# Performance work log

Measured on AMD Instinct MI355X. Metric: run time of the kernel, lower is better.

## Reference

```python
import jax, jax.numpy as jnp
import numpy as np

N, E, G = 50000, 800000, 64          # nodes, edges, graphs in batch
F, HG, HL = 64, 128, 128             # node feat, graph hidden, lin hidden
AVG_LOG = float(np.log(9.0))         # from deg histogram [0]*8+[1]: log(8+1)


def setup_inputs() -> dict:
    key = jax.random.key(0)
    ks = jax.random.split(key, 24)
    def w(k, shape):
        return 0.1 * jax.random.normal(k, shape, jnp.float32)
    return {
        "x": jax.random.normal(ks[0], (N, F), jnp.float32),
        "edge_index": jax.random.randint(ks[1], (2, E), 0, N),
        "edge_attr": jax.random.normal(ks[2], (E, 1), jnp.float32),
        "batch": jnp.sort(jax.random.randint(ks[3], (N,), 0, G)),
        # PNAConv params (towers=1, pre_layers=1, post_layers=1, edge_dim=1)
        "W_edge": w(ks[4], (1, F)),      "b_edge": w(ks[5], (F,)),
        "W_pre": w(ks[6], (3 * F, F)),   "b_pre": w(ks[7], (F,)),
        "W_post": w(ks[8], (13 * F, HG)), "b_post": w(ks[9], (HG,)),
        "W_lin": w(ks[10], (HG, HG)),    "b_lin": w(ks[11], (HG,)),
        # bn1 / fc2 / bn2
        "g1": jnp.ones((HG,)), "be1": jnp.zeros((HG,)),
        "W2": w(ks[12], (HG, HL)), "b2": w(ks[13], (HL,)),
        "g2": jnp.ones((HL,)), "be2": jnp.zeros((HL,)),
        # one resnet block: fc/bn/fc/bn
        "Wr1": w(ks[14], (HL, HL)), "br1": w(ks[15], (HL,)),
        "gr1": jnp.ones((HL,)), "ber1": jnp.zeros((HL,)),
        "Wr2": w(ks[16], (HL, HL)), "br2": w(ks[17], (HL,)),
        "gr2": jnp.ones((HL,)), "ber2": jnp.zeros((HL,)),
        "W_out": w(ks[18], (HL, 1)), "b_out": w(ks[19], (1,)),
    }


def _bn(z, g, b):
    # BatchNorm1d, training mode: biased batch stats, eps=1e-5
    mu = z.mean(0)
    var = ((z - mu) ** 2).mean(0)
    return (z - mu) * jax.lax.rsqrt(var + 1e-5) * g + b


def _pna(x, edge_index, edge_attr, W_edge, b_edge, W_pre, b_pre,
         W_post, b_post, W_lin, b_lin):
    src, dst = edge_index[0], edge_index[1]  # messages flow j->i, aggregate at dst
    e = edge_attr @ W_edge + b_edge                               # [E, F]
    m = jnp.concatenate([x[dst], x[src], e], -1) @ W_pre + b_pre  # [E, F]
    ones_e = jnp.ones((m.shape[0],), m.dtype)
    cnt = jax.ops.segment_sum(ones_e, dst, N)                     # in-degree
    cnt1 = jnp.maximum(cnt, 1.0)
    mean = jax.ops.segment_sum(m, dst, N) / cnt1[:, None]
    mean2 = jax.ops.segment_sum(m * m, dst, N) / cnt1[:, None]
    std = jnp.sqrt(jax.nn.relu(mean2 - mean * mean) + 1e-5)
    has = (cnt > 0)[:, None]
    mn = jnp.where(has, jax.ops.segment_min(m, dst, N), 0.0)
    mx = jnp.where(has, jax.ops.segment_max(m, dst, N), 0.0)
    agg = jnp.concatenate([mean, mn, mx, std], -1)                # [N, 4F]
    amp = (jnp.log(cnt1 + 1.0) / AVG_LOG)[:, None]                # amplification scaler
    out = jnp.concatenate([agg, agg * amp, agg / amp], -1)        # [N, 12F]
    out = jnp.concatenate([x, out], -1) @ W_post + b_post         # [N, HG]
    return out @ W_lin + b_lin                                    # [N, HG]


def reference(x, edge_index, edge_attr, batch,
              W_edge, b_edge, W_pre, b_pre, W_post, b_post, W_lin, b_lin,
              g1, be1, W2, b2, g2, be2,
              Wr1, br1, gr1, ber1, Wr2, br2, gr2, ber2,
              W_out, b_out):
    h = _pna(x, edge_index, edge_attr, W_edge, b_edge, W_pre, b_pre,
             W_post, b_post, W_lin, b_lin)
    # global_mean_pool over graphs
    gc = jnp.maximum(jax.ops.segment_sum(jnp.ones((h.shape[0],), h.dtype), batch, G), 1.0)
    z = jax.ops.segment_sum(h, batch, G) / gc[:, None]            # [G, HG]
    z = jax.nn.relu(_bn(z, g1, be1))
    z = jax.nn.relu(_bn(z @ W2 + b2, g2, be2))
    r = z
    z = jax.nn.relu(_bn(z @ Wr1 + br1, gr1, ber1))
    z = jax.nn.relu(_bn(z @ Wr2 + br2, gr2, ber2) + r)
    return z @ W_out + b_out                                      # [G, 1]
```

## Files before the change

kernel.cpp:

```cpp
#include <hip/hip_runtime.h>
#include <hip/hip_bf16.h>

using bf16 = __hip_bfloat16;

#define F 64
#define HG 128
#define HL 128
#define AVG_LOG_INV 0.45511961331341866f
#define BSH 5
#define BNODES 32
#define BCAP 1024
#define BTILE 8192
#define NBMAX 1664

typedef short short8 __attribute__((ext_vector_type(8)));
typedef float floatx4 __attribute__((ext_vector_type(4)));

__device__ __forceinline__ float b2f(bf16 v) { return __bfloat162float(v); }
__device__ __forceinline__ bf16 f2b(float v) { return __float2bfloat16(v); }
__device__ __forceinline__ short f2bs(float v) { bf16 h = f2b(v); return *(short*)&h; }

__device__ __forceinline__ unsigned packbf2(float x, float y) {
    bf16 a = f2b(x), b = f2b(y);
    unsigned short ua = *(unsigned short*)&a, ub = *(unsigned short*)&b;
    return ((unsigned)ub << 16) | (unsigned)ua;
}

__device__ __forceinline__ float wave_sum(float v) {
    #pragma unroll
    for (int m = 32; m > 0; m >>= 1) v += __shfl_xor(v, m);
    return v;
}

__global__ void k_ab_mfma(const float* __restrict__ x, const float* __restrict__ W_pre,
                          bf16* __restrict__ AB, int N,
                          int* __restrict__ gcur, float* __restrict__ gfeat,
                          int* __restrict__ gcnt, int NB, int GF, int G,
                          const float* __restrict__ W_edge, const float* __restrict__ b_edge,
                          const float* __restrict__ b_pre, float* __restrict__ uc) {
    int gtid = blockIdx.x * blockDim.x + threadIdx.x;
    int gstr = gridDim.x * blockDim.x;
    for (int i = gtid; i < GF; i += gstr) gfeat[i] = 0.f;
    for (int i = gtid; i < NB; i += gstr) gcur[i] = 0;
    for (int i = gtid; i < G; i += gstr) gcnt[i] = 0;
    if (blockIdx.x == 0 && threadIdx.x < 64) {
        int f = threadIdx.x;
        float u = 0.f, c = b_pre[f];
        for (int k = 0; k < 64; k++) {
            float w3 = W_pre[(128 + k) * 64 + f];
            u += W_edge[k] * w3;
            c += b_edge[k] * w3;
        }
        uc[f] = u; uc[64 + f] = c;
    }

    __shared__ unsigned short wt[128 * 72];
    for (int idx = threadIdx.x; idx < 8192; idx += 256) {
        int k = idx >> 7, m = idx & 127;
        float v = W_pre[((m & 64) + k) * 64 + (m & 63)];
        wt[m * 72 + k] = (unsigned short)f2bs(v);
    }
    __syncthreads();

    int lane = threadIdx.x & 63;
    int row = lane & 15, quad = lane >> 4;
    int w = (blockIdx.x * blockDim.x + threadIdx.x) >> 6;
    int nwaves = (gridDim.x * blockDim.x) >> 6;
    int ntiles = (N + 15) >> 4;

    for (int tile = w; tile < ntiles; tile += nwaves) {
        int m0 = tile << 4;
        int node_a = m0 + row; if (node_a >= N) node_a = N - 1;
        short8 a[2];
        #pragma unroll
        for (int h = 0; h < 2; h++) {
            const float* xp = x + (size_t)node_a * 64 + h * 32 + quad * 8;
            floatx4 v0 = *(const floatx4*)xp;
            floatx4 v1 = *(const floatx4*)(xp + 4);
            #pragma unroll
            for (int j = 0; j < 4; j++) { a[h][j] = f2bs(v0[j]); a[h][4 + j] = f2bs(v1[j]); }
        }
        #pragma unroll
        for (int t = 0; t < 8; t++) {
            int fbase = t * 16;
            floatx4 c = {0.f, 0.f, 0.f, 0.f};
            #pragma unroll
            for (int h = 0; h < 2; h++) {
                short8 b = *(const short8*)(wt + (fbase + row) * 72 + h * 32 + quad * 8);
                c = __builtin_amdgcn_mfma_f32_16x16x32_bf16(a[h], b, c, 0, 0, 0);
            }
            #pragma unroll
            for (int r = 0; r < 4; r++) {
                int node = m0 + quad * 4 + r;
                if (node < N) AB[(size_t)node * 128 + fbase + row] = f2b(c[r]);
            }
        }
    }
}

__global__ void k_bucket(const int* __restrict__ ei, const float* __restrict__ ea,
                         int* __restrict__ gcur, int2* __restrict__ gout,
                         int E, int NB) {
    __shared__ int2 recs[BTILE];
    __shared__ int hist[NBMAX], gst[NBMAX], lrk[NBMAX];
    int t = threadIdx.x;
    for (int b = t; b < NB; b += 1024) hist[b] = 0;
    __syncthreads();
    int base = blockIdx.x * BTILE;
    int lim = E - base; if (lim > BTILE) lim = BTILE;
    int nq = lim >> 2;
    const int4* src4 = (const int4*)(ei + base);
    const int4* dst4 = (const int4*)(ei + E + base);
    const float4* ea4 = (const float4*)(ea + base);
    for (int q = t; q < nq; q += 1024) {
        int4 s = src4[q], d = dst4[q];
        float4 v = ea4[q];
        int i = q * 4;
        recs[i]     = make_int2((d.x << 16) | s.x, __float_as_int(v.x));
        recs[i + 1] = make_int2((d.y << 16) | s.y, __float_as_int(v.y));
        recs[i + 2] = make_int2((d.z << 16) | s.z, __float_as_int(v.z));
        recs[i + 3] = make_int2((d.w << 16) | s.w, __float_as_int(v.w));
        atomicAdd(&hist[d.x >> BSH], 1);
        atomicAdd(&hist[d.y >> BSH], 1);
        atomicAdd(&hist[d.z >> BSH], 1);
        atomicAdd(&hist[d.w >> BSH], 1);
    }
    for (int i = (nq << 2) + t; i < lim; i += 1024) {
        int e = base + i;
        int src = ei[e], dst = ei[E + e];
        recs[i] = make_int2((dst << 16) | src, __float_as_int(ea[e]));
        atomicAdd(&hist[dst >> BSH], 1);
    }
    __syncthreads();
    for (int b = t; b < NB; b += 1024) {
        int h = hist[b];
        lrk[b] = 0;
        gst[b] = (h > 0) ? atomicAdd(&gcur[b], h) : 0;
    }
    __syncthreads();
    for (int i = t; i < lim; i += 1024) {
        int2 r = recs[i];
        int b = ((unsigned)r.x) >> (16 + BSH);
        int k = atomicAdd(&lrk[b], 1);
        int pos = gst[b] + k;
        if (pos < BCAP) gout[(size_t)b * BCAP + pos] = r;
    }
}

__global__ void k_edge(const bf16* __restrict__ AB, const int2* __restrict__ gout,
                       const int* __restrict__ gcur, const float* __restrict__ uc,
                       const int* __restrict__ batch, float* __restrict__ gfeat,
                       int N) {
    __shared__ int2 recs[BCAP], sortd[BCAP];
    __shared__ int ncnt[BNODES], nofs[BNODES], nrank[BNODES];
    __shared__ int gid[BNODES];
    __shared__ unsigned lstat[BNODES][128];
    __shared__ float lamp[BNODES], liamp[BNODES];
    int t = threadIdx.x;
    int b = blockIdx.x;
    int nn = N - b * BNODES; if (nn > BNODES) nn = BNODES;
    int ecnt = gcur[b]; if (ecnt > BCAP) ecnt = BCAP;

    for (int i = t; i < ecnt; i += 512) recs[i] = gout[(size_t)b * BCAP + i];
    if (t < BNODES) {
        ncnt[t] = 0; nrank[t] = 0;
        if (t < nn) gid[t] = batch[b * BNODES + t];
    }
    __syncthreads();
    for (int i = t; i < ecnt; i += 512)
        atomicAdd(&ncnt[((unsigned)recs[i].x >> 16) & (BNODES - 1)], 1);
    __syncthreads();
    if (t < BNODES) {
        int v = ncnt[t], inc = v;
        #pragma unroll
        for (int m = 1; m < BNODES; m <<= 1) { int u = __shfl_up(inc, m); if (t >= m) inc += u; }
        nofs[t] = inc - v;
    }
    __syncthreads();
    for (int i = t; i < ecnt; i += 512) {
        int2 r = recs[i];
        int nl = ((unsigned)r.x >> 16) & (BNODES - 1);
        int k = atomicAdd(&nrank[nl], 1);
        sortd[nofs[nl] + k] = r;
    }
    __syncthreads();

    int lane = t & 63, w = t >> 6;
    int half = lane & 31, hi32 = lane >> 5;
    float2 u2 = *(const float2*)(uc + 2 * half);
    float2 c2 = *(const float2*)(uc + 64 + 2 * half);

    for (int nl = w; nl < nn; nl += 8) {
        int n = b * BNODES + nl;
        int lo = nofs[nl], cnt = ncnt[nl], hi = lo + cnt;

        unsigned apack = *(const unsigned*)(AB + (size_t)n * 128 + 2 * half);
        float acx = __uint_as_float(apack << 16) + c2.x;
        float acy = __uint_as_float(apack & 0xffff0000u) + c2.y;

        float sx = 0.f, sy = 0.f, qx = 0.f, qy = 0.f;
        float mnx = 3.4e38f, mny = 3.4e38f, mxx = -3.4e38f, mxy = -3.4e38f;

        auto acc2 = [&](unsigned bp, float eav) {
            float bx = __uint_as_float(bp << 16);
            float by = __uint_as_float(bp & 0xffff0000u);
            float m0 = fmaf(eav, u2.x, acx) + bx;
            float m1 = fmaf(eav, u2.y, acy) + by;
            sx += m0; qx = fmaf(m0, m0, qx);
            sy += m1; qy = fmaf(m1, m1, qy);
            mnx = fminf(mnx, m0); mxx = fmaxf(mxx, m0);
            mny = fminf(mny, m1); mxy = fmaxf(mxy, m1);
        };
        auto gaddr = [&](int sn) {
            return (const unsigned*)(AB + (size_t)sn * 128 + 64 + 2 * half);
        };

        for (int base = lo; base < hi; base += 64) {
            int nb = hi - base; if (nb > 64) nb = 64;
            int2 rec = (lane < nb) ? sortd[base + lane] : make_int2(0, 0);
            int vsn = rec.x & 0xFFFF;
            float vea = __int_as_float(rec.y);
            int i = 0;
            for (; i + 8 <= nb; i += 8) {
                int sn0 = __shfl(vsn, i + hi32);
                int sn1 = __shfl(vsn, i + 2 + hi32);
                int sn2 = __shfl(vsn, i + 4 + hi32);
                int sn3 = __shfl(vsn, i + 6 + hi32);
                float e0 = __shfl(vea, i + hi32);
                float e1 = __shfl(vea, i + 2 + hi32);
                float e2 = __shfl(vea, i + 4 + hi32);
                float e3 = __shfl(vea, i + 6 + hi32);
                unsigned b0 = *gaddr(sn0);
                unsigned b1 = *gaddr(sn1);
                unsigned b2 = *gaddr(sn2);
                unsigned b3 = *gaddr(sn3);
                acc2(b0, e0); acc2(b1, e1); acc2(b2, e2); acc2(b3, e3);
            }
            for (; i + 2 <= nb; i += 2) {
                int   sn = __shfl(vsn, i + hi32);
                float ev = __shfl(vea, i + hi32);
                acc2(*gaddr(sn), ev);
            }
            if (i < nb) {
                int   sn = __shfl(vsn, i);
                float ev = __shfl(vea, i);
                unsigned bp = *gaddr(sn);
                if (hi32 == 0) acc2(bp, ev);
            }
        }
        sx += __shfl_xor(sx, 32); sy += __shfl_xor(sy, 32);
        qx += __shfl_xor(qx, 32); qy += __shfl_xor(qy, 32);
        mnx = fminf(mnx, __shfl_xor(mnx, 32)); mny = fminf(mny, __shfl_xor(mny, 32));
        mxx = fmaxf(mxx, __shfl_xor(mxx, 32)); mxy = fmaxf(mxy, __shfl_xor(mxy, 32));

        float c1 = (cnt > 0) ? (float)cnt : 1.f;
        float inv = 1.f / c1;
        float mex = sx * inv, mey = sy * inv;
        float vx = qx * inv - mex * mex; if (vx < 0.f) vx = 0.f;
        float vy = qy * inv - mey * mey; if (vy < 0.f) vy = 0.f;
        float sdx = sqrtf(vx + 1e-5f), sdy = sqrtf(vy + 1e-5f);
        if (cnt == 0) { mnx = mny = mxx = mxy = 0.f; }

        if (hi32 == 0) {
            lstat[nl][half]      = packbf2(mex, mey);
            lstat[nl][32 + half] = packbf2(mnx, mny);
        } else {
            lstat[nl][64 + half] = packbf2(mxx, mxy);
            lstat[nl][96 + half] = packbf2(sdx, sdy);
        }
        if (lane == 0) {
            float amp = logf(c1 + 1.f) * AVG_LOG_INV;
            lamp[nl] = amp; liamp[nl] = 1.f / amp;
        }
    }
    __syncthreads();

    if (t < 128) {
        int c = t;
        int elem = ((c >> 5) << 6) + ((c & 31) << 1);
        float s1x = 0.f, s1y = 0.f, s2x = 0.f, s2y = 0.f, s3x = 0.f, s3y = 0.f;
        int cur = gid[0];
        for (int nl = 0; nl < nn; nl++) {
            int g = gid[nl];
            if (g != cur) {
                float* gf = gfeat + (size_t)cur * 832;
                unsafeAtomicAdd(&gf[64 + elem], s1x);
                unsafeAtomicAdd(&gf[65 + elem], s1y);
                unsafeAtomicAdd(&gf[320 + elem], s2x);
                unsafeAtomicAdd(&gf[321 + elem], s2y);
                unsafeAtomicAdd(&gf[576 + elem], s3x);
                unsafeAtomicAdd(&gf[577 + elem], s3y);
                s1x = s1y = s2x = s2y = s3x = s3y = 0.f;
                cur = g;
            }
            unsigned p = lstat[nl][c];
            float bx = __uint_as_float(p << 16);
            float by = __uint_as_float(p & 0xffff0000u);
            float a = lamp[nl], ia = liamp[nl];
            s1x += bx; s2x = fmaf(bx, a, s2x); s3x = fmaf(bx, ia, s3x);
            s1y += by; s2y = fmaf(by, a, s2y); s3y = fmaf(by, ia, s3y);
        }
        float* gf = gfeat + (size_t)cur * 832;
        unsafeAtomicAdd(&gf[64 + elem], s1x);
        unsafeAtomicAdd(&gf[65 + elem], s1y);
        unsafeAtomicAdd(&gf[320 + elem], s2x);
        unsafeAtomicAdd(&gf[321 + elem], s2y);
        unsafeAtomicAdd(&gf[576 + elem], s3x);
        unsafeAtomicAdd(&gf[577 + elem], s3y);
    }
}

__global__ void k_gx(const float* __restrict__ x, const int* __restrict__ batch,
                     float* __restrict__ gfeat, int* __restrict__ gcnt,
                     int N, int chunk) {
    int t = threadIdx.x;
    int lo = blockIdx.x * chunk;
    int hi = lo + chunk; if (hi > N) hi = N;
    if (lo >= hi) return;
    int curg = batch[lo];
    float sx = 0.f;
    int cnt = 0;
    for (int n = lo; n < hi; n++) {
        int g = batch[n];
        if (g != curg) {
            unsafeAtomicAdd(&gfeat[(size_t)curg * 832 + t], sx);
            if (t == 0) atomicAdd(&gcnt[curg], cnt);
            sx = 0.f; cnt = 0; curg = g;
        }
        sx += x[(size_t)n * 64 + t];
        cnt++;
    }
    unsafeAtomicAdd(&gfeat[(size_t)curg * 832 + t], sx);
    if (t == 0) atomicAdd(&gcnt[curg], cnt);
}

__global__ void k_post1(const float* __restrict__ gfeat, const int* __restrict__ gcnt,
                        const float* __restrict__ W_post, const float* __restrict__ b_post,
                        const float* __restrict__ W_lin, const float* __restrict__ b_lin,
                        float* __restrict__ Zin) {
    int g = blockIdx.x, j = threadIdx.x;
    __shared__ float feat[832];
    __shared__ float z1[128];
    int cg = gcnt[g];
    float r = 1.f / ((cg > 0) ? (float)cg : 1.f);
    for (int i = j; i < 832; i += 128) feat[i] = gfeat[(size_t)g * 832 + i] * r;
    __syncthreads();
    float acc = b_post[j];
    for (int k = 0; k < 832; k++) acc += feat[k] * W_post[k * 128 + j];
    z1[j] = acc;
    __syncthreads();
    float a2 = b_lin[j];
    for (int k = 0; k < 128; k++) a2 += z1[k] * W_lin[k * 128 + j];
    if (cg == 0) a2 = 0.f;
    Zin[g * 128 + j] = a2;
}

__global__ void k_mlpcol(const float* __restrict__ in, const float* __restrict__ W,
                         const float* __restrict__ bias,
                         const float* __restrict__ gamma, const float* __restrict__ beta,
                         const float* __restrict__ res,
                         const float* __restrict__ g_in, const float* __restrict__ be_in,
                         float* __restrict__ outp) {
    __shared__ float A[64 * 129];
    __shared__ float part[4 * 64];
    int t = threadIdx.x;
    int j = blockIdx.x;

    for (int i = t; i < 8192; i += 256) A[(i >> 7) * 129 + (i & 127)] = in[i];
    __syncthreads();

    if (g_in) {
        if (t < 128) {
            int c = t;
            float mu = 0.f;
            for (int r = 0; r < 64; r++) mu += A[r * 129 + c];
            mu *= (1.f / 64.f);
            float var = 0.f;
            for (int r = 0; r < 64; r++) { float d = A[r * 129 + c] - mu; var += d * d; }
            var *= (1.f / 64.f);
            float sc = rsqrtf(var + 1e-5f) * g_in[c], sh = be_in[c];
            for (int r = 0; r < 64; r++) {
                float v = (A[r * 129 + c] - mu) * sc + sh;
                A[r * 129 + c] = v > 0.f ? v : 0.f;
            }
        }
        __syncthreads();
    }

    int r = t & 63, q = t >> 6;
    float acc = 0.f;
    int k0 = q * 32;
    #pragma unroll
    for (int k = 0; k < 32; k++) acc += A[r * 129 + k0 + k] * W[(k0 + k) * 128 + j];
    part[q * 64 + r] = acc;
    __syncthreads();

    if (t < 64) {
        float v = part[t] + part[64 + t] + part[128 + t] + part[192 + t] + bias[j];
        float mu = wave_sum(v) * (1.f / 64.f);
        float d = v - mu;
        float var = wave_sum(d * d) * (1.f / 64.f);
        float o = d * rsqrtf(var + 1e-5f) * gamma[j] + beta[j];
        if (res) o += res[t * 128 + j];
        outp[t * 128 + j] = o > 0.f ? o : 0.f;
    }
}

__global__ void k_out(const float* __restrict__ z4, const float* __restrict__ W_out,
                      const float* b_out, float* __restrict__ out) {
    int g = threadIdx.x;
    float acc = b_out[0];
    for (int j = 0; j < 128; j++) acc += z4[g * 128 + j] * W_out[j];
    out[g] = acc;
}

extern "C" void kernel_launch(void* const* d_in, const int* in_sizes, int n_in,
                              void* d_out, int out_size, void* d_ws, size_t ws_size,
                              hipStream_t stream) {
    const float* x      = (const float*)d_in[0];
    const int*   ei     = (const int*)d_in[1];
    const float* ea     = (const float*)d_in[2];
    const int*   batch  = (const int*)d_in[3];
    const float* W_edge = (const float*)d_in[4];
    const float* b_edge = (const float*)d_in[5];
    const float* W_pre  = (const float*)d_in[6];
    const float* b_pre  = (const float*)d_in[7];
    const float* W_post = (const float*)d_in[8];
    const float* b_post = (const float*)d_in[9];
    const float* W_lin  = (const float*)d_in[10];
    const float* b_lin  = (const float*)d_in[11];
    const float* g1     = (const float*)d_in[12];
    const float* be1    = (const float*)d_in[13];
    const float* W2     = (const float*)d_in[14];
    const float* b2     = (const float*)d_in[15];
    const float* g2     = (const float*)d_in[16];
    const float* be2    = (const float*)d_in[17];
    const float* Wr1    = (const float*)d_in[18];
    const float* br1    = (const float*)d_in[19];
    const float* gr1    = (const float*)d_in[20];
    const float* ber1   = (const float*)d_in[21];
    const float* Wr2    = (const float*)d_in[22];
    const float* br2    = (const float*)d_in[23];
    const float* gr2    = (const float*)d_in[24];
    const float* ber2   = (const float*)d_in[25];
    const float* W_out  = (const float*)d_in[26];
    const float* b_out  = (const float*)d_in[27];
    float* out = (float*)d_out;

    const int N = in_sizes[0] / F;
    const int E = in_sizes[1] / 2;
    const int G = out_size;
    const int NB = (N + BNODES - 1) >> BSH;

    char* p = (char*)d_ws;
    auto alloc = [&](size_t nbytes) { void* r = p; p += (nbytes + 255) & ~(size_t)255; return r; };
    bf16*  AB     = (bf16*)alloc((size_t)N * 128 * sizeof(bf16));
    int*   gcur   = (int*)alloc((size_t)NB * sizeof(int));
    int2*  gout   = (int2*)alloc((size_t)NB * BCAP * sizeof(int2));
    float* uc     = (float*)alloc(128 * sizeof(float));
    float* gfeat  = (float*)alloc((size_t)G * 832 * sizeof(float));
    int*   gcnt   = (int*)alloc((size_t)G * sizeof(int));
    float* Zin    = (float*)alloc(64 * 128 * sizeof(float));
    float* z2b    = (float*)alloc(64 * 128 * sizeof(float));
    float* z3b    = (float*)alloc(64 * 128 * sizeof(float));
    float* z4b    = (float*)alloc(64 * 128 * sizeof(float));

    const int GF = G * 832;
    const int GXB = 2048;
    const int GXCH = (N + GXB - 1) / GXB;
    const int ABB = ((N + 15) / 16 + 3) / 4;
    const int NBT = (E + BTILE - 1) / BTILE;

    k_ab_mfma<<<ABB, 256, 0, stream>>>(x, W_pre, AB, N, gcur, gfeat, gcnt, NB, GF, G,
                                       W_edge, b_edge, b_pre, uc);
    k_bucket<<<NBT, 1024, 0, stream>>>(ei, ea, gcur, gout, E, NB);
    k_edge<<<NB, 512, 0, stream>>>(AB, gout, gcur, uc, batch, gfeat, N);
    k_gx<<<GXB, 64, 0, stream>>>(x, batch, gfeat, gcnt, N, GXCH);
    k_post1<<<G, 128, 0, stream>>>(gfeat, gcnt, W_post, b_post, W_lin, b_lin, Zin);
    k_mlpcol<<<HG, 256, 0, stream>>>(Zin, W2, b2, g2, be2, nullptr, g1, be1, z2b);
    k_mlpcol<<<HL, 256, 0, stream>>>(z2b, Wr1, br1, gr1, ber1, nullptr, nullptr, nullptr, z3b);
    k_mlpcol<<<HL, 256, 0, stream>>>(z3b, Wr2, br2, gr2, ber2, z2b, nullptr, nullptr, z4b);
    k_out<<<1, 64, 0, stream>>>(z4b, W_out, b_out, out);
}
```

Baseline: 237.0 us.

## Fuse bucketing with AB matmul, drop global atomics, fold graph-x pooling into edge kernel

```diff
diff --git a/kernel.cpp b/kernel.cpp
--- a/kernel.cpp
+++ b/kernel.cpp
@@ -12,6 +12,7 @@
 #define BCAP 1024
 #define BTILE 8192
 #define NBMAX 1664
+#define NBTMAX 128
 
 typedef short short8 __attribute__((ext_vector_type(8)));
 typedef float floatx4 __attribute__((ext_vector_type(4)));
@@ -32,139 +33,197 @@
     return v;
 }
 
-__global__ void k_ab_mfma(const float* __restrict__ x, const float* __restrict__ W_pre,
-                          bf16* __restrict__ AB, int N,
-                          int* __restrict__ gcur, float* __restrict__ gfeat,
-                          int* __restrict__ gcnt, int NB, int GF, int G,
-                          const float* __restrict__ W_edge, const float* __restrict__ b_edge,
-                          const float* __restrict__ b_pre, float* __restrict__ uc) {
-    int gtid = blockIdx.x * blockDim.x + threadIdx.x;
-    int gstr = gridDim.x * blockDim.x;
+__global__ __launch_bounds__(512) void k_prep(
+    const float* __restrict__ x, const float* __restrict__ W_pre,
+    bf16* __restrict__ AB, int N,
+    const int* __restrict__ ei, const float* __restrict__ ea,
+    int* __restrict__ ofs, int2* __restrict__ gout, int E,
+    float* __restrict__ gfeat, int* __restrict__ gcnt,
+    int NB, int GF, int G, int NBT,
+    const float* __restrict__ W_edge, const float* __restrict__ b_edge,
+    const float* __restrict__ b_pre, float* __restrict__ uc) {
+    __shared__ __align__(16) char smem[18432];
+    int t = threadIdx.x;
+    int gtid = blockIdx.x * 512 + t;
+    int gstr = gridDim.x * 512;
     for (int i = gtid; i < GF; i += gstr) gfeat[i] = 0.f;
-    for (int i = gtid; i < NB; i += gstr) gcur[i] = 0;
     for (int i = gtid; i < G; i += gstr) gcnt[i] = 0;
-    if (blockIdx.x == 0 && threadIdx.x < 64) {
-        int f = threadIdx.x;
-        float u = 0.f, c = b_pre[f];
-        for (int k = 0; k < 64; k++) {
-            float w3 = W_pre[(128 + k) * 64 + f];
-            u += W_edge[k] * w3;
-            c += b_edge[k] * w3;
-        }
-        uc[f] = u; uc[64 + f] = c;
-    }
-
-    __shared__ unsigned short wt[128 * 72];
-    for (int idx = threadIdx.x; idx < 8192; idx += 256) {
-        int k = idx >> 7, m = idx & 127;
-        float v = W_pre[((m & 64) + k) * 64 + (m & 63)];
-        wt[m * 72 + k] = (unsigned short)f2bs(v);
-    }
-    __syncthreads();
-
-    int lane = threadIdx.x & 63;
-    int row = lane & 15, quad = lane >> 4;
-    int w = (blockIdx.x * blockDim.x + threadIdx.x) >> 6;
-    int nwaves = (gridDim.x * blockDim.x) >> 6;
-    int ntiles = (N + 15) >> 4;
-
-    for (int tile = w; tile < ntiles; tile += nwaves) {
-        int m0 = tile << 4;
-        int node_a = m0 + row; if (node_a >= N) node_a = N - 1;
-        short8 a[2];
-        #pragma unroll
-        for (int h = 0; h < 2; h++) {
-            const float* xp = x + (size_t)node_a * 64 + h * 32 + quad * 8;
-            floatx4 v0 = *(const floatx4*)xp;
-            floatx4 v1 = *(const floatx4*)(xp + 4);
-            #pragma unroll
-            for (int j = 0; j < 4; j++) { a[h][j] = f2bs(v0[j]); a[h][4 + j] = f2bs(v1[j]); }
-        }
-        #pragma unroll
-        for (int t = 0; t < 8; t++) {
-            int fbase = t * 16;
-            floatx4 c = {0.f, 0.f, 0.f, 0.f};
+
+    if (blockIdx.x < NBT) {
+        int* hist = (int*)smem;
+        int* aux  = hist + NBMAX;
+        int p = blockIdx.x;
+        for (int i = t; i < NB; i += 512) hist[i] = 0;
+        __syncthreads();
+        int base = p * BTILE;
+        int lim = E - base; if (lim > BTILE) lim = BTILE;
+        int nq = lim >> 2;
+        const int4* dst4 = (const int4*)(ei + E + base);
+        for (int q = t; q < nq; q += 512) {
+            int4 d = dst4[q];
+            atomicAdd(&hist[d.x >> BSH], 1);
+            atomicAdd(&hist[d.y >> BSH], 1);
+            atomicAdd(&hist[d.z >> BSH], 1);
+            atomicAdd(&hist[d.w >> BSH], 1);
+        }
+        for (int i = (nq << 2) + t; i < lim; i += 512)
+            atomicAdd(&hist[ei[E + base + i] >> BSH], 1);
+        __syncthreads();
+        int b0 = t * 4;
+        int c0 = 0, c1 = 0, c2 = 0, c3 = 0;
+        if (b0 < NB)     c0 = hist[b0];
+        if (b0 + 1 < NB) c1 = hist[b0 + 1];
+        if (b0 + 2 < NB) c2 = hist[b0 + 2];
+        if (b0 + 3 < NB) c3 = hist[b0 + 3];
+        int tot = c0 + c1 + c2 + c3;
+        aux[t] = tot;
+        __syncthreads();
+        for (int d = 1; d < 512; d <<= 1) {
+            int v = (t >= d) ? aux[t - d] : 0;
+            __syncthreads();
+            aux[t] += v;
+            __syncthreads();
+        }
+        int run = aux[t] - tot;
+        __syncthreads();
+        size_t orow = (size_t)p * (NB + 1);
+        if (b0 < NB)     { hist[b0]     = run; ofs[orow + b0]     = run; run += c0; }
+        if (b0 + 1 < NB) { hist[b0 + 1] = run; ofs[orow + b0 + 1] = run; run += c1; }
+        if (b0 + 2 < NB) { hist[b0 + 2] = run; ofs[orow + b0 + 2] = run; run += c2; }
+        if (b0 + 3 < NB) { hist[b0 + 3] = run; ofs[orow + b0 + 3] = run; run += c3; }
+        if (t == 0) ofs[orow + NB] = lim;
+        for (int i = t; i < NB; i += 512) aux[i] = 0;
+        __syncthreads();
+        const int4* src4 = (const int4*)(ei + base);
+        const float4* ea4 = (const float4*)(ea + base);
+        int2* seg = gout + (size_t)p * BTILE;
+        for (int q = t; q < nq; q += 512) {
+            int4 s = src4[q], d = dst4[q];
+            float4 v = ea4[q];
+            int bb, pos;
+            bb = d.x >> BSH; pos = hist[bb] + atomicAdd(&aux[bb], 1);
+            seg[pos] = make_int2((d.x << 16) | s.x, __float_as_int(v.x));
+            bb = d.y >> BSH; pos = hist[bb] + atomicAdd(&aux[bb], 1);
+            seg[pos] = make_int2((d.y << 16) | s.y, __float_as_int(v.y));
+            bb = d.z >> BSH; pos = hist[bb] + atomicAdd(&aux[bb], 1);
+            seg[pos] = make_int2((d.z << 16) | s.z, __float_as_int(v.z));
+            bb = d.w >> BSH; pos = hist[bb] + atomicAdd(&aux[bb], 1);
+            seg[pos] = make_int2((d.w << 16) | s.w, __float_as_int(v.w));
+        }
+        for (int i = (nq << 2) + t; i < lim; i += 512) {
+            int s = ei[base + i], d = ei[E + base + i];
+            int bb = d >> BSH;
+            int pos = hist[bb] + atomicAdd(&aux[bb], 1);
+            seg[pos] = make_int2((d << 16) | s, __float_as_int(ea[base + i]));
+        }
+    } else {
+        if (blockIdx.x == NBT && t < 64) {
+            int f = t;
+            float u = 0.f, c = b_pre[f];
+            for (int k = 0; k < 64; k++) {
+                float w3 = W_pre[(128 + k) * 64 + f];
+                u += W_edge[k] * w3;
+                c += b_edge[k] * w3;
+            }
+            uc[f] = u; uc[64 + f] = c;
+        }
+        unsigned short* wt = (unsigned short*)smem;
+        for (int idx = t; idx < 8192; idx += 512) {
+            int k = idx >> 7, m = idx & 127;
+            float v = W_pre[((m & 64) + k) * 64 + (m & 63)];
+            wt[m * 72 + k] = (unsigned short)f2bs(v);
+        }
+        __syncthreads();
+
+        int lane = t & 63;
+        int row = lane & 15, quad = lane >> 4;
+        int w = (blockIdx.x - NBT) * 8 + (t >> 6);
+        int nwaves = (gridDim.x - NBT) * 8;
+        int ntiles = (N + 15) >> 4;
+
+        for (int tile = w; tile < ntiles; tile += nwaves) {
+            int m0 = tile << 4;
+            int node_a = m0 + row; if (node_a >= N) node_a = N - 1;
+            short8 a[2];
             #pragma unroll
             for (int h = 0; h < 2; h++) {
-                short8 b = *(const short8*)(wt + (fbase + row) * 72 + h * 32 + quad * 8);
-                c = __builtin_amdgcn_mfma_f32_16x16x32_bf16(a[h], b, c, 0, 0, 0);
+                const float* xp = x + (size_t)node_a * 64 + h * 32 + quad * 8;
+                floatx4 v0 = *(const floatx4*)xp;
+                floatx4 v1 = *(const floatx4*)(xp + 4);
+                #pragma unroll
+                for (int j = 0; j < 4; j++) { a[h][j] = f2bs(v0[j]); a[h][4 + j] = f2bs(v1[j]); }
             }
             #pragma unroll
-            for (int r = 0; r < 4; r++) {
-                int node = m0 + quad * 4 + r;
-                if (node < N) AB[(size_t)node * 128 + fbase + row] = f2b(c[r]);
-            }
-        }
-    }
-}
-
-__global__ void k_bucket(const int* __restrict__ ei, const float* __restrict__ ea,
-                         int* __restrict__ gcur, int2* __restrict__ gout,
-                         int E, int NB) {
-    __shared__ int2 recs[BTILE];
-    __shared__ int hist[NBMAX], gst[NBMAX], lrk[NBMAX];
-    int t = threadIdx.x;
-    for (int b = t; b < NB; b += 1024) hist[b] = 0;
-    __syncthreads();
-    int base = blockIdx.x * BTILE;
-    int lim = E - base; if (lim > BTILE) lim = BTILE;
-    int nq = lim >> 2;
-    const int4* src4 = (const int4*)(ei + base);
-    const int4* dst4 = (const int4*)(ei + E + base);
-    const float4* ea4 = (const float4*)(ea + base);
-    for (int q = t; q < nq; q += 1024) {
-        int4 s = src4[q], d = dst4[q];
-        float4 v = ea4[q];
-        int i = q * 4;
-        recs[i]     = make_int2((d.x << 16) | s.x, __float_as_int(v.x));
-        recs[i + 1] = make_int2((d.y << 16) | s.y, __float_as_int(v.y));
-        recs[i + 2] = make_int2((d.z << 16) | s.z, __float_as_int(v.z));
-        recs[i + 3] = make_int2((d.w << 16) | s.w, __float_as_int(v.w));
-        atomicAdd(&hist[d.x >> BSH], 1);
-        atomicAdd(&hist[d.y >> BSH], 1);
-        atomicAdd(&hist[d.z >> BSH], 1);
-        atomicAdd(&hist[d.w >> BSH], 1);
-    }
-    for (int i = (nq << 2) + t; i < lim; i += 1024) {
-        int e = base + i;
-        int src = ei[e], dst = ei[E + e];
-        recs[i] = make_int2((dst << 16) | src, __float_as_int(ea[e]));
-        atomicAdd(&hist[dst >> BSH], 1);
-    }
-    __syncthreads();
-    for (int b = t; b < NB; b += 1024) {
-        int h = hist[b];
-        lrk[b] = 0;
-        gst[b] = (h > 0) ? atomicAdd(&gcur[b], h) : 0;
-    }
-    __syncthreads();
-    for (int i = t; i < lim; i += 1024) {
-        int2 r = recs[i];
-        int b = ((unsigned)r.x) >> (16 + BSH);
-        int k = atomicAdd(&lrk[b], 1);
-        int pos = gst[b] + k;
-        if (pos < BCAP) gout[(size_t)b * BCAP + pos] = r;
-    }
-}
-
-__global__ void k_edge(const bf16* __restrict__ AB, const int2* __restrict__ gout,
-                       const int* __restrict__ gcur, const float* __restrict__ uc,
-                       const int* __restrict__ batch, float* __restrict__ gfeat,
-                       int N) {
+            for (int tt = 0; tt < 8; tt++) {
+                int fbase = tt * 16;
+                floatx4 c = {0.f, 0.f, 0.f, 0.f};
+                #pragma unroll
+                for (int h = 0; h < 2; h++) {
+                    short8 bfr = *(const short8*)(wt + (fbase + row) * 72 + h * 32 + quad * 8);
+                    c = __builtin_amdgcn_mfma_f32_16x16x32_bf16(a[h], bfr, c, 0, 0, 0);
+                }
+                #pragma unroll
+                for (int r = 0; r < 4; r++) {
+                    int node = m0 + quad * 4 + r;
+                    if (node < N) AB[(size_t)node * 128 + fbase + row] = f2b(c[r]);
+                }
+            }
+        }
+    }
+}
+
+__global__ __launch_bounds__(512) void k_edge(
+    const bf16* __restrict__ AB, const int2* __restrict__ gout,
+    const int* __restrict__ ofs, const float* __restrict__ uc,
+    const int* __restrict__ batch, const float* __restrict__ x,
+    float* __restrict__ gfeat, int* __restrict__ gcnt,
+    int N, int NB, int NBT) {
     __shared__ int2 recs[BCAP], sortd[BCAP];
     __shared__ int ncnt[BNODES], nofs[BNODES], nrank[BNODES];
     __shared__ int gid[BNODES];
     __shared__ unsigned lstat[BNODES][128];
     __shared__ float lamp[BNODES], liamp[BNODES];
+    __shared__ int runlo[NBTMAX], runlen[NBTMAX], runpre[NBTMAX];
+    __shared__ int etot_s;
     int t = threadIdx.x;
     int b = blockIdx.x;
     int nn = N - b * BNODES; if (nn > BNODES) nn = BNODES;
-    int ecnt = gcur[b]; if (ecnt > BCAP) ecnt = BCAP;
-
-    for (int i = t; i < ecnt; i += 512) recs[i] = gout[(size_t)b * BCAP + i];
+
+    if (t < NBTMAX) { runlo[t] = 0; runlen[t] = 0; }
     if (t < BNODES) {
         ncnt[t] = 0; nrank[t] = 0;
         if (t < nn) gid[t] = batch[b * BNODES + t];
+    }
+    __syncthreads();
+    if (t < NBT) {
+        int lo = ofs[(size_t)t * (NB + 1) + b];
+        int hi = ofs[(size_t)t * (NB + 1) + b + 1];
+        runlo[t] = lo; runlen[t] = hi - lo;
+    }
+    __syncthreads();
+    if (t < NBTMAX) runpre[t] = runlen[t];
+    __syncthreads();
+    for (int d = 1; d < NBTMAX; d <<= 1) {
+        int v = 0;
+        if (t < NBTMAX && t >= d) v = runpre[t - d];
+        __syncthreads();
+        if (t < NBTMAX) runpre[t] += v;
+        __syncthreads();
+    }
+    if (t == NBTMAX - 1) etot_s = runpre[NBTMAX - 1];
+    int ex = 0;
+    if (t < NBTMAX) ex = runpre[t] - runlen[t];
+    __syncthreads();
+    if (t < NBTMAX) runpre[t] = ex;
+    __syncthreads();
+    int ecnt = etot_s; if (ecnt > BCAP) ecnt = BCAP;
+    for (int i = t; i < ecnt; i += 512) {
+        int lo2 = 0, hi2 = NBT;
+        while (hi2 - lo2 > 1) {
+            int mid = (lo2 + hi2) >> 1;
+            if (runpre[mid] <= i) lo2 = mid; else hi2 = mid;
+        }
+        recs[i] = gout[(size_t)lo2 * BTILE + runlo[lo2] + (i - runpre[lo2])];
     }
     __syncthreads();
     for (int i = t; i < ecnt; i += 512)
@@ -279,6 +338,8 @@
         int c = t;
         int elem = ((c >> 5) << 6) + ((c & 31) << 1);
         float s1x = 0.f, s1y = 0.f, s2x = 0.f, s2y = 0.f, s3x = 0.f, s3y = 0.f;
+        float sxv = 0.f;
+        int cnt = 0;
         int cur = gid[0];
         for (int nl = 0; nl < nn; nl++) {
             int g = gid[nl];
@@ -290,7 +351,9 @@
                 unsafeAtomicAdd(&gf[321 + elem], s2y);
                 unsafeAtomicAdd(&gf[576 + elem], s3x);
                 unsafeAtomicAdd(&gf[577 + elem], s3y);
-                s1x = s1y = s2x = s2y = s3x = s3y = 0.f;
+                if (t < 64) unsafeAtomicAdd(&gf[t], sxv);
+                if (t == 0) atomicAdd(&gcnt[cur], cnt);
+                s1x = s1y = s2x = s2y = s3x = s3y = 0.f; sxv = 0.f; cnt = 0;
                 cur = g;
             }
             unsigned p = lstat[nl][c];
@@ -299,6 +362,8 @@
             float a = lamp[nl], ia = liamp[nl];
             s1x += bx; s2x = fmaf(bx, a, s2x); s3x = fmaf(bx, ia, s3x);
             s1y += by; s2y = fmaf(by, a, s2y); s3y = fmaf(by, ia, s3y);
+            if (t < 64) sxv += x[(size_t)(b * BNODES + nl) * 64 + t];
+            cnt++;
         }
         float* gf = gfeat + (size_t)cur * 832;
         unsafeAtomicAdd(&gf[64 + elem], s1x);
@@ -307,52 +372,43 @@
         unsafeAtomicAdd(&gf[321 + elem], s2y);
         unsafeAtomicAdd(&gf[576 + elem], s3x);
         unsafeAtomicAdd(&gf[577 + elem], s3y);
-    }
-}
-
-__global__ void k_gx(const float* __restrict__ x, const int* __restrict__ batch,
-                     float* __restrict__ gfeat, int* __restrict__ gcnt,
-                     int N, int chunk) {
-    int t = threadIdx.x;
-    int lo = blockIdx.x * chunk;
-    int hi = lo + chunk; if (hi > N) hi = N;
-    if (lo >= hi) return;
-    int curg = batch[lo];
-    float sx = 0.f;
-    int cnt = 0;
-    for (int n = lo; n < hi; n++) {
-        int g = batch[n];
-        if (g != curg) {
-            unsafeAtomicAdd(&gfeat[(size_t)curg * 832 + t], sx);
-            if (t == 0) atomicAdd(&gcnt[curg], cnt);
-            sx = 0.f; cnt = 0; curg = g;
-        }
-        sx += x[(size_t)n * 64 + t];
-        cnt++;
-    }
-    unsafeAtomicAdd(&gfeat[(size_t)curg * 832 + t], sx);
-    if (t == 0) atomicAdd(&gcnt[curg], cnt);
+        if (t < 64) unsafeAtomicAdd(&gf[t], sxv);
+        if (t == 0) atomicAdd(&gcnt[cur], cnt);
+    }
 }
 
 __global__ void k_post1(const float* __restrict__ gfeat, const int* __restrict__ gcnt,
                         const float* __restrict__ W_post, const float* __restrict__ b_post,
                         const float* __restrict__ W_lin, const float* __restrict__ b_lin,
                         float* __restrict__ Zin) {
-    int g = blockIdx.x, j = threadIdx.x;
+    int g = blockIdx.x, t = threadIdx.x;
+    int j = t & 127, h = t >> 7;
     __shared__ float feat[832];
+    __shared__ float part[256];
     __shared__ float z1[128];
     int cg = gcnt[g];
     float r = 1.f / ((cg > 0) ? (float)cg : 1.f);
-    for (int i = j; i < 832; i += 128) feat[i] = gfeat[(size_t)g * 832 + i] * r;
-    __syncthreads();
-    float acc = b_post[j];
-    for (int k = 0; k < 832; k++) acc += feat[k] * W_post[k * 128 + j];
-    z1[j] = acc;
-    __syncthreads();
-    float a2 = b_lin[j];
-    for (int k = 0; k < 128; k++) a2 += z1[k] * W_lin[k * 128 + j];
-    if (cg == 0) a2 = 0.f;
-    Zin[g * 128 + j] = a2;
+    for (int i = t; i < 832; i += 256) feat[i] = gfeat[(size_t)g * 832 + i] * r;
+    __syncthreads();
+    float acc = (h == 0) ? b_post[j] : 0.f;
+    const float* Wp = W_post + (size_t)(h * 416) * 128 + j;
+    const float* fp = feat + h * 416;
+    #pragma unroll 8
+    for (int k = 0; k < 416; k++) acc += fp[k] * Wp[(size_t)k * 128];
+    part[t] = acc;
+    __syncthreads();
+    if (t < 128) z1[j] = part[j] + part[128 + j];
+    __syncthreads();
+    float a2 = (h == 0) ? b_lin[j] : 0.f;
+    #pragma unroll
+    for (int k = 0; k < 64; k++) a2 += z1[h * 64 + k] * W_lin[(h * 64 + k) * 128 + j];
+    part[t] = a2;
+    __syncthreads();
+    if (t < 128) {
+        float v = part[j] + part[128 + j];
+        if (cg == 0) v = 0.f;
+        Zin[g * 128 + j] = v;
+    }
 }
 
 __global__ void k_mlpcol(const float* __restrict__ in, const float* __restrict__ W,
@@ -454,9 +510,10 @@
 
     char* p = (char*)d_ws;
     auto alloc = [&](size_t nbytes) { void* r = p; p += (nbytes + 255) & ~(size_t)255; return r; };
+    const int NBT = (E + BTILE - 1) / BTILE;
     bf16*  AB     = (bf16*)alloc((size_t)N * 128 * sizeof(bf16));
-    int*   gcur   = (int*)alloc((size_t)NB * sizeof(int));
-    int2*  gout   = (int2*)alloc((size_t)NB * BCAP * sizeof(int2));
+    int2*  gout   = (int2*)alloc((size_t)NBT * BTILE * sizeof(int2));
+    int*   ofs    = (int*)alloc((size_t)NBT * (NB + 1) * sizeof(int));
     float* uc     = (float*)alloc(128 * sizeof(float));
     float* gfeat  = (float*)alloc((size_t)G * 832 * sizeof(float));
     int*   gcnt   = (int*)alloc((size_t)G * sizeof(int));
@@ -466,17 +523,13 @@
     float* z4b    = (float*)alloc(64 * 128 * sizeof(float));
 
     const int GF = G * 832;
-    const int GXB = 2048;
-    const int GXCH = (N + GXB - 1) / GXB;
-    const int ABB = ((N + 15) / 16 + 3) / 4;
-    const int NBT = (E + BTILE - 1) / BTILE;
-
-    k_ab_mfma<<<ABB, 256, 0, stream>>>(x, W_pre, AB, N, gcur, gfeat, gcnt, NB, GF, G,
-                                       W_edge, b_edge, b_pre, uc);
-    k_bucket<<<NBT, 1024, 0, stream>>>(ei, ea, gcur, gout, E, NB);
-    k_edge<<<NB, 512, 0, stream>>>(AB, gout, gcur, uc, batch, gfeat, N);
-    k_gx<<<GXB, 64, 0, stream>>>(x, batch, gfeat, gcnt, N, GXCH);
-    k_post1<<<G, 128, 0, stream>>>(gfeat, gcnt, W_post, b_post, W_lin, b_lin, Zin);
+    const int NAB = (((N + 15) >> 4) + 7) >> 3;
+
+    k_prep<<<NBT + NAB, 512, 0, stream>>>(x, W_pre, AB, N, ei, ea, ofs, gout, E,
+                                          gfeat, gcnt, NB, GF, G, NBT,
+                                          W_edge, b_edge, b_pre, uc);
+    k_edge<<<NB, 512, 0, stream>>>(AB, gout, ofs, uc, batch, x, gfeat, gcnt, N, NB, NBT);
+    k_post1<<<G, 256, 0, stream>>>(gfeat, gcnt, W_post, b_post, W_lin, b_lin, Zin);
     k_mlpcol<<<HG, 256, 0, stream>>>(Zin, W2, b2, g2, be2, nullptr, g1, be1, z2b);
     k_mlpcol<<<HL, 256, 0, stream>>>(z2b, Wr1, br1, gr1, ber1, nullptr, nullptr, nullptr, z3b);
     k_mlpcol<<<HL, 256, 0, stream>>>(z3b, Wr2, br2, gr2, ber2, z2b, nullptr, nullptr, z4b);
```

New measurement: 227.0 us. 1.04x faster.
